# Performance work log

Hardware: AMD Instinct MI355X
Metric: run time of the kernel (lower is better)

Reference implementation:

```python
import jax, jax.numpy as jnp
import numpy as np

S, B, T = 512, 256, 128


def setup_inputs() -> dict:
    key = jax.random.key(0)
    k1, k2, k3, k4, k5, k6 = jax.random.split(key, 6)
    emissions = jax.random.normal(k1, (S, B, T), dtype=jnp.float32)
    # realistic monotone mask: each sequence has a random length in [1, S]
    lengths = jax.random.randint(k2, (B,), 1, S + 1)
    mask = (jnp.arange(S)[:, None] < lengths[None, :]).astype(jnp.float32)  # [S,B]
    tags = jax.random.randint(k3, (S, B), 0, T)
    transitions = jax.random.normal(k4, (T, T), dtype=jnp.float32)
    start_transitions = jax.random.normal(k5, (T,), dtype=jnp.float32)
    stop_transitions = jax.random.normal(k6, (T,), dtype=jnp.float32)
    return {
        "emissions": emissions,
        "mask": mask,
        "tags": tags,
        "transitions": transitions,
        "start_transitions": start_transitions,
        "stop_transitions": stop_transitions,
    }


def reference(emissions, mask, tags, transitions, start_transitions, stop_transitions):
    seq_len, batch, num_tags = emissions.shape

    # ---- log-partition (forward algorithm) + viterbi score, fused scan ----
    init = start_transitions + emissions[0]  # [B,T]

    def part_step(carry, xs):
        fv, vv = carry  # forward var, viterbi var: [B,T]
        em, m = xs      # em: [B,T], m: [B]
        # scores[b, j, k] = em[b, j] + transitions[j, k]  (j=next tag, k=prev tag)
        scores = em[:, :, None] + transitions[None, :, :]          # [B,T,T]
        lse = jax.nn.logsumexp(fv[:, None, :] + scores, axis=2)     # [B,T]
        vmax = jnp.max(vv[:, None, :] + scores, axis=2)             # [B,T]
        fv = m[:, None] * lse + (1.0 - m)[:, None] * fv
        vv = m[:, None] * vmax + (1.0 - m)[:, None] * vv
        return (fv, vv), None

    (fv, vv), _ = jax.lax.scan(part_step, (init, init), (emissions[1:], mask[1:]))
    total_score = jax.nn.logsumexp(fv + stop_transitions, axis=1)   # [B]
    best_path_score = jnp.max(vv + stop_transitions, axis=1)        # [B]

    # ---- gold path score ----
    barange = jnp.arange(batch)
    tag0 = tags[0]
    rps0 = start_transitions[tag0] + emissions[0, barange, tag0] * mask[0]

    def rp_step(carry, xs):
        rps, prev = carry
        cur, em, m = xs  # cur:[B] int, em:[B,T], m:[B]
        rps = rps + transitions[prev, cur] * m
        rps = rps + jnp.take_along_axis(em, cur[:, None], axis=1)[:, 0] * m
        prev = jnp.where(m == 1.0, cur, prev)
        return (rps, prev), None

    (rps, prev), _ = jax.lax.scan(rp_step, (rps0, tag0), (tags[1:], emissions[1:], mask[1:]))
    real_path_score = rps + stop_transitions[prev]

    loss = jnp.mean(total_score - real_path_score)
    return loss, real_path_score, total_score, best_path_score
```

## Files before the change

### kernel.cpp

```cpp
#include <hip/hip_runtime.h>
#include <math.h>

#define S_LEN 512
#define BATCH 256
#define NTAG  128
#define EMSTRIDE (BATCH * NTAG)

typedef float f32x4 __attribute__((ext_vector_type(4)));
typedef float f32x2 __attribute__((ext_vector_type(2)));

__device__ __forceinline__ int lidx(int k) { return k + ((k >> 6) << 2); }
__device__ __forceinline__ f32x2 lo2(f32x4 v){ f32x2 r; r[0]=v[0]; r[1]=v[1]; return r; }
__device__ __forceinline__ f32x2 hi2(f32x4 v){ f32x2 r; r[0]=v[2]; r[1]=v[3]; return r; }
__device__ __forceinline__ f32x2 pmax2(f32x2 a, f32x2 b){
  f32x2 r; r[0]=fmaxf(a[0],b[0]); r[1]=fmaxf(a[1],b[1]); return r;
}

#define DPP_XOR1(x) __int_as_float(__builtin_amdgcn_mov_dpp(__float_as_int(x), 0xB1, 0xF, 0xF, false))

#define BAR() do {                                       \
    asm volatile("s_waitcnt lgkmcnt(0)" ::: "memory");   \
    __builtin_amdgcn_s_barrier();                        \
    __builtin_amdgcn_sched_barrier(0);                   \
  } while (0)

__global__ __launch_bounds__(256, 1)
void crf_fat_kernel(const float* __restrict__ emis,
                    const float* __restrict__ mask,
                    const int* __restrict__ tags,
                    const float* __restrict__ trans,
                    const float* __restrict__ startt,
                    const float* __restrict__ stopt,
                    float* __restrict__ ws,
                    int* __restrict__ ewbuf,
                    float* __restrict__ out)
{
  const int blk  = blockIdx.x;
  const int tid  = threadIdx.x;
  const int role = blk >> 8;
  const int b    = blk & 255;
  const int lane = tid & 63;
  const int wid  = tid >> 6;

  __shared__ __align__(16) float sbuf[2][144];
  __shared__ float red[8];

  if (role == 4) {
    float part = 0.f, lenp = 0.f;
#pragma unroll
    for (int rep = 0; rep < 2; ++rep) {
      int s = tid + rep * 256;
      float m  = mask[(size_t)s * BATCH + b];
      int  cur = tags[(size_t)s * BATCH + b];
      if (s == 0) {
        part += startt[cur] + emis[(size_t)b * NTAG + cur] * m;
      } else {
        int prev = tags[(size_t)(s - 1) * BATCH + b];
        part += m * (trans[(size_t)prev * NTAG + cur] +
                     emis[((size_t)s * BATCH + b) * NTAG + cur]);
      }
      lenp += m;
    }
#pragma unroll
    for (int d = 1; d <= 32; d <<= 1) {
      part += __shfl_xor(part, d);
      lenp += __shfl_xor(lenp, d);
    }
    if (lane == 0) { red[wid] = part; red[4 + wid] = lenp; }
    __syncthreads();
    if (tid == 0) {
      float rps = (red[0] + red[1]) + (red[2] + red[3]);
      float lf  = (red[4] + red[5]) + (red[6] + red[7]);
      int len = (int)(lf + 0.5f);
      int pf  = tags[(size_t)(len - 1) * BATCH + b];
      out[1 + b] = rps + stopt[pf];
    }
    return;
  }

  const int p    = tid >> 1;
  const int h    = tid & 1;
  const int widx = lidx(p);

  int len;
  {
    float mv = mask[(size_t)tid * BATCH + b] +
               mask[(size_t)(tid + 256) * BATCH + b];
#pragma unroll
    for (int d = 1; d <= 32; d <<= 1) mv += __shfl_xor(mv, d);
    if (lane == 0) red[wid] = mv;
    __syncthreads();
    float ls = (red[0] + red[1]) + (red[2] + red[3]);
    len = (int)(ls + 0.5f);
    len = __builtin_amdgcn_readfirstlane(len);
  }
  const int sm     = (len - 1) >> 1;
  const int nsteps = len - 1 - sm;
  const float* eb  = emis + (size_t)b * NTAG + p;

  if (role == 0) {
    f32x2 E2[32];
    {
      const float* tr = trans + (size_t)p * NTAG + 64 * h;
#pragma unroll
      for (int c = 0; c < 16; ++c) {
        f32x4 t = *(const f32x4*)(tr + 4 * c);
        f32x2 a, bb;
        a[0] = __expf(t[0]); a[1] = __expf(t[1]);
        bb[0] = __expf(t[2]); bb[1] = __expf(t[3]);
        E2[2*c] = a; E2[2*c+1] = bb;
      }
    }
    if (h == 0) sbuf[0][widx] = __expf(startt[p] + eb[0]);
    float e0 = eb[(size_t)1 * EMSTRIDE];
    float e1 = eb[(size_t)2 * EMSTRIDE];
    float e2 = eb[(size_t)3 * EMSTRIDE];
    float e3 = eb[(size_t)4 * EMSTRIDE];
    int Ew = 0, fin = 0;
    __syncthreads();

#define FSTEP(U, EXV, RENORM)                                                 \
  {                                                                           \
    if (g + (U) > sm) { fin = (U) & 1; goto epi_f; }                          \
    const f32x4* wr = (const f32x4*)(sbuf[(U) & 1] + 68 * h);                 \
    f32x2 a0 = {0.f, 0.f}, a1 = {0.f, 0.f}, r2 = {0.f, 0.f};                  \
    _Pragma("unroll")                                                         \
    for (int c = 0; c < 16; ++c) {                                            \
      f32x4 w = wr[c];                                                        \
      f32x2 wl = lo2(w), wh = hi2(w);                                         \
      a0 = a0 + E2[2*c] * wl;                                                 \
      a1 = a1 + E2[2*c+1] * wh;                                               \
      if (RENORM) r2 = pmax2(r2, pmax2(wl, wh));                              \
    }                                                                         \
    f32x2 as = a0 + a1;                                                       \
    float sum = as[0] + as[1];                                                \
    sum += DPP_XOR1(sum);                                                     \
    float uf;                                                                 \
    if (RENORM) {                                                             \
      float rw = fmaxf(r2[0], r2[1]);                                         \
      rw = fmaxf(rw, DPP_XOR1(rw));                                           \
      int ew = (int)((__float_as_uint(rw) >> 23) & 0xFF) - 126;               \
      Ew += ew;                                                               \
      float swc = __uint_as_float((unsigned)(127 - ew) << 23);                \
      uf = (EXV) * sum * swc;                                                 \
    } else {                                                                  \
      uf = (EXV) * sum;                                                       \
    }                                                                         \
    if (h == 0) sbuf[((U) + 1) & 1][widx] = uf;                               \
    BAR();                                                                    \
  }

    for (int g = 1; g < S_LEN; g += 4) {
      int c0 = g + 4 < S_LEN ? g + 4 : S_LEN - 1;
      int c1 = g + 5 < S_LEN ? g + 5 : S_LEN - 1;
      int c2 = g + 6 < S_LEN ? g + 6 : S_LEN - 1;
      int c3 = g + 7 < S_LEN ? g + 7 : S_LEN - 1;
      float n0 = eb[(size_t)c0 * EMSTRIDE];
      float n1 = eb[(size_t)c1 * EMSTRIDE];
      float n2 = eb[(size_t)c2 * EMSTRIDE];
      float n3 = eb[(size_t)c3 * EMSTRIDE];
      float x0 = __expf(e0), x1 = __expf(e1);
      float x2 = __expf(e2), x3 = __expf(e3);
      FSTEP(0, x0, 0)
      FSTEP(1, x1, 0)
      FSTEP(2, x2, 0)
      FSTEP(3, x3, 1)
      e0 = n0; e1 = n1; e2 = n2; e3 = n3;
    }
    fin = 0;
epi_f:
    {
      if (tid < 128) ws[(size_t)b * 512 + tid] = sbuf[fin][lidx(tid)];
      if (tid == 0) ewbuf[b] = Ew;
    }
  } else if (role == 1) {
    f32x2 E2[32];
    {
      const float* tc = trans + p + (size_t)(64 * h) * NTAG;
#pragma unroll
      for (int e = 0; e < 32; ++e) {
        f32x2 a;
        a[0] = __expf(tc[(size_t)(2*e)     * NTAG]);
        a[1] = __expf(tc[(size_t)(2*e + 1) * NTAG]);
        E2[e] = a;
      }
    }
    if (h == 0) {
      float st = stopt[p];
      float y = (nsteps > 0) ? __expf(st + eb[(size_t)(len - 1) * EMSTRIDE])
                             : __expf(st);
      sbuf[0][widx] = y;
    }
    int s0i = len - 2;     s0i = s0i < 0 ? 0 : s0i;
    int s1i = len - 3;     s1i = s1i < 0 ? 0 : s1i;
    int s2i = len - 4;     s2i = s2i < 0 ? 0 : s2i;
    int s3i = len - 5;     s3i = s3i < 0 ? 0 : s3i;
    float e0 = eb[(size_t)s0i * EMSTRIDE];
    float e1 = eb[(size_t)s1i * EMSTRIDE];
    float e2 = eb[(size_t)s2i * EMSTRIDE];
    float e3 = eb[(size_t)s3i * EMSTRIDE];
    int Ew = 0, fin = 0;
    __syncthreads();

#define BSTEP(U, EXV, RENORM)                                                 \
  {                                                                           \
    if (gi + (U) >= nsteps) { fin = (U) & 1; goto epi_b; }                    \
    const f32x4* wr = (const f32x4*)(sbuf[(U) & 1] + 68 * h);                 \
    f32x2 a0 = {0.f, 0.f}, a1 = {0.f, 0.f}, r2 = {0.f, 0.f};                  \
    _Pragma("unroll")                                                         \
    for (int c = 0; c < 16; ++c) {                                            \
      f32x4 w = wr[c];                                                        \
      f32x2 wl = lo2(w), wh = hi2(w);                                         \
      a0 = a0 + E2[2*c] * wl;                                                 \
      a1 = a1 + E2[2*c+1] * wh;                                               \
      if (RENORM) r2 = pmax2(r2, pmax2(wl, wh));                              \
    }                                                                         \
    f32x2 as = a0 + a1;                                                       \
    float sum = as[0] + as[1];                                                \
    sum += DPP_XOR1(sum);                                                     \
    float exm = (gi + (U) == nsteps - 1) ? 1.0f : (EXV);                      \
    float uf;                                                                 \
    if (RENORM) {                                                             \
      float rw = fmaxf(r2[0], r2[1]);                                         \
      rw = fmaxf(rw, DPP_XOR1(rw));                                           \
      int ew = (int)((__float_as_uint(rw) >> 23) & 0xFF) - 126;               \
      Ew += ew;                                                               \
      float swc = __uint_as_float((unsigned)(127 - ew) << 23);                \
      uf = exm * sum * swc;                                                   \
    } else {                                                                  \
      uf = exm * sum;                                                         \
    }                                                                         \
    if (h == 0) sbuf[((U) + 1) & 1][widx] = uf;                               \
    BAR();                                                                    \
  }

    for (int gi = 0; gi < S_LEN; gi += 4) {
      int c0 = len - 2 - (gi + 4); c0 = c0 < 0 ? 0 : c0;
      int c1 = len - 2 - (gi + 5); c1 = c1 < 0 ? 0 : c1;
      int c2 = len - 2 - (gi + 6); c2 = c2 < 0 ? 0 : c2;
      int c3 = len - 2 - (gi + 7); c3 = c3 < 0 ? 0 : c3;
      float n0 = eb[(size_t)c0 * EMSTRIDE];
      float n1 = eb[(size_t)c1 * EMSTRIDE];
      float n2 = eb[(size_t)c2 * EMSTRIDE];
      float n3 = eb[(size_t)c3 * EMSTRIDE];
      float x0 = __expf(e0), x1 = __expf(e1);
      float x2 = __expf(e2), x3 = __expf(e3);
      BSTEP(0, x0, 0)
      BSTEP(1, x1, 0)
      BSTEP(2, x2, 0)
      BSTEP(3, x3, 1)
      e0 = n0; e1 = n1; e2 = n2; e3 = n3;
    }
    fin = 0;
epi_b:
    {
      if (tid < 128) ws[(size_t)b * 512 + 128 + tid] = sbuf[fin][lidx(tid)];
      if (tid == 0) ewbuf[BATCH + b] = Ew;
    }
  } else if (role == 2) {
    f32x2 T2[32];
    {
      const float* tr = trans + (size_t)p * NTAG + 64 * h;
#pragma unroll
      for (int c = 0; c < 16; ++c) {
        f32x4 t = *(const f32x4*)(tr + 4 * c);
        T2[2*c]   = lo2(t);
        T2[2*c+1] = hi2(t);
      }
    }
    if (h == 0) sbuf[0][widx] = startt[p] + eb[0];
    float e0 = eb[(size_t)1 * EMSTRIDE];
    float e1 = eb[(size_t)2 * EMSTRIDE];
    float e2 = eb[(size_t)3 * EMSTRIDE];
    float e3 = eb[(size_t)4 * EMSTRIDE];
    int fin = 0;
    __syncthreads();

#define VSTEP(U, EMV)                                                         \
  {                                                                           \
    if (g + (U) > sm) { fin = (U) & 1; goto epi_v; }                          \
    const f32x4* vr = (const f32x4*)(sbuf[(U) & 1] + 68 * h);                 \
    f32x2 m2 = {-3.0e38f, -3.0e38f};                                          \
    _Pragma("unroll")                                                         \
    for (int c = 0; c < 16; ++c) {                                            \
      f32x4 v = vr[c];                                                        \
      m2 = pmax2(m2, pmax2(lo2(v) + T2[2*c], hi2(v) + T2[2*c+1]));            \
    }                                                                         \
    float vm = fmaxf(m2[0], m2[1]);                                           \
    vm = fmaxf(vm, DPP_XOR1(vm));                                             \
    float uv = (EMV) + vm;                                                    \
    if (h == 0) sbuf[((U) + 1) & 1][widx] = uv;                               \
    BAR();                                                                    \
  }

    for (int g = 1; g < S_LEN; g += 4) {
      int c0 = g + 4 < S_LEN ? g + 4 : S_LEN - 1;
      int c1 = g + 5 < S_LEN ? g + 5 : S_LEN - 1;
      int c2 = g + 6 < S_LEN ? g + 6 : S_LEN - 1;
      int c3 = g + 7 < S_LEN ? g + 7 : S_LEN - 1;
      float n0 = eb[(size_t)c0 * EMSTRIDE];
      float n1 = eb[(size_t)c1 * EMSTRIDE];
      float n2 = eb[(size_t)c2 * EMSTRIDE];
      float n3 = eb[(size_t)c3 * EMSTRIDE];
      VSTEP(0, e0)
      VSTEP(1, e1)
      VSTEP(2, e2)
      VSTEP(3, e3)
      e0 = n0; e1 = n1; e2 = n2; e3 = n3;
    }
    fin = 0;
epi_v:
    {
      if (tid < 128) ws[(size_t)b * 512 + 256 + tid] = sbuf[fin][lidx(tid)];
    }
  } else {
    f32x2 T2[32];
    {
      const float* tc = trans + p + (size_t)(64 * h) * NTAG;
#pragma unroll
      for (int e = 0; e < 32; ++e) {
        f32x2 a;
        a[0] = tc[(size_t)(2*e)     * NTAG];
        a[1] = tc[(size_t)(2*e + 1) * NTAG];
        T2[e] = a;
      }
    }
    if (h == 0) {
      float st = stopt[p];
      float y = (nsteps > 0) ? st + eb[(size_t)(len - 1) * EMSTRIDE] : st;
      sbuf[0][widx] = y;
    }
    int s0i = len - 2;     s0i = s0i < 0 ? 0 : s0i;
    int s1i = len - 3;     s1i = s1i < 0 ? 0 : s1i;
    int s2i = len - 4;     s2i = s2i < 0 ? 0 : s2i;
    int s3i = len - 5;     s3i = s3i < 0 ? 0 : s3i;
    float e0 = eb[(size_t)s0i * EMSTRIDE];
    float e1 = eb[(size_t)s1i * EMSTRIDE];
    float e2 = eb[(size_t)s2i * EMSTRIDE];
    float e3 = eb[(size_t)s3i * EMSTRIDE];
    int fin = 0;
    __syncthreads();

#define WSTEP(U, EMV)                                                         \
  {                                                                           \
    if (gi + (U) >= nsteps) { fin = (U) & 1; goto epi_w; }                    \
    const f32x4* vr = (const f32x4*)(sbuf[(U) & 1] + 68 * h);                 \
    f32x2 m2 = {-3.0e38f, -3.0e38f};                                          \
    _Pragma("unroll")                                                         \
    for (int c = 0; c < 16; ++c) {                                            \
      f32x4 v = vr[c];                                                        \
      m2 = pmax2(m2, pmax2(lo2(v) + T2[2*c], hi2(v) + T2[2*c+1]));            \
    }                                                                         \
    float vm = fmaxf(m2[0], m2[1]);                                           \
    vm = fmaxf(vm, DPP_XOR1(vm));                                             \
    float uv = (gi + (U) == nsteps - 1) ? vm : vm + (EMV);                    \
    if (h == 0) sbuf[((U) + 1) & 1][widx] = uv;                               \
    BAR();                                                                    \
  }

    for (int gi = 0; gi < S_LEN; gi += 4) {
      int c0 = len - 2 - (gi + 4); c0 = c0 < 0 ? 0 : c0;
      int c1 = len - 2 - (gi + 5); c1 = c1 < 0 ? 0 : c1;
      int c2 = len - 2 - (gi + 6); c2 = c2 < 0 ? 0 : c2;
      int c3 = len - 2 - (gi + 7); c3 = c3 < 0 ? 0 : c3;
      float n0 = eb[(size_t)c0 * EMSTRIDE];
      float n1 = eb[(size_t)c1 * EMSTRIDE];
      float n2 = eb[(size_t)c2 * EMSTRIDE];
      float n3 = eb[(size_t)c3 * EMSTRIDE];
      WSTEP(0, e0)
      WSTEP(1, e1)
      WSTEP(2, e2)
      WSTEP(3, e3)
      e0 = n0; e1 = n1; e2 = n2; e3 = n3;
    }
    fin = 0;
epi_w:
    {
      if (tid < 128) ws[(size_t)b * 512 + 384 + tid] = sbuf[fin][lidx(tid)];
    }
  }
}

__global__ __launch_bounds__(128, 1)
void crf_combine_kernel(const float* __restrict__ ws,
                        const int* __restrict__ ewbuf,
                        float* __restrict__ out)
{
  const int b = blockIdx.x, k = threadIdx.x;
  const float* base = ws + (size_t)b * 512;
  float t1 = base[k] * base[128 + k];
  float m1 = base[256 + k] + base[384 + k];
#pragma unroll
  for (int d = 1; d <= 32; d <<= 1) {
    t1 += __shfl_xor(t1, d);
    m1 = fmaxf(m1, __shfl_xor(m1, d));
  }
  __shared__ float rs[2], rm[2];
  const int lane = k & 63, wid = k >> 6;
  if (lane == 0) { rs[wid] = t1; rm[wid] = m1; }
  __syncthreads();
  if (k == 0) {
    const double LN2 = 0.6931471805599453;
    int Et = ewbuf[b] + ewbuf[BATCH + b];
    out[1 + BATCH + b]     = (float)((double)Et * LN2 + (double)__logf(rs[0] + rs[1]));
    out[1 + 2 * BATCH + b] = fmaxf(rm[0], rm[1]);
  }
}

__global__ __launch_bounds__(256, 1)
void crf_loss_kernel(float* __restrict__ out)
{
  const int tid = threadIdx.x;
  float dft = out[1 + BATCH + tid] - out[1 + tid];
#pragma unroll
  for (int d = 1; d <= 32; d <<= 1) dft += __shfl_xor(dft, d);
  __shared__ float rs[4];
  const int lane = tid & 63, wid = tid >> 6;
  if (lane == 0) rs[wid] = dft;
  __syncthreads();
  if (tid == 0)
    out[0] = ((rs[0] + rs[1]) + (rs[2] + rs[3])) * (1.0f / BATCH);
}

extern "C" void kernel_launch(void* const* d_in, const int* in_sizes, int n_in,
                              void* d_out, int out_size, void* d_ws, size_t ws_size,
                              hipStream_t stream)
{
  const float* emis   = (const float*)d_in[0];
  const float* mask   = (const float*)d_in[1];
  const int*   tags   = (const int*)d_in[2];
  const float* trans  = (const float*)d_in[3];
  const float* startt = (const float*)d_in[4];
  const float* stopt  = (const float*)d_in[5];
  float* out = (float*)d_out;

  float* wsf   = (float*)d_ws;
  int*   ewbuf = (int*)(wsf + 512 * BATCH);

  crf_fat_kernel<<<5 * BATCH, 256, 0, stream>>>(emis, mask, tags, trans,
                                                startt, stopt, wsf, ewbuf, out);
  crf_combine_kernel<<<BATCH, 128, 0, stream>>>(wsf, ewbuf, out);
  crf_loss_kernel<<<1, 256, 0, stream>>>(out);
}
```

Measured before the change: 210.0 us.

## Shrink recurrence blocks to 128 threads, each lane computing four output tags

Each recurrence block now runs two wavefronts instead of four. Every thread computes partial sums for four output tags over a 32-wide slice of the previous tags, reduces across four lanes with two DPP steps, and selects its own result, so every thread writes one tag per step instead of half the threads idling on the write. The shared-memory padding layout is changed to fit 32-element chunks, and the inner products use explicit FMAs. The intent is to make the per-step barrier cheaper with fewer waves and to reuse each LDS read across four outputs. The cost is more registers per thread (four transition rows held at once) and extra DPP reduction and select work on every step.

New measurement: 213.0 us. No clear change (+1.4%).

```diff
diff --git a/kernel.cpp b/kernel.cpp
--- a/kernel.cpp
+++ b/kernel.cpp
@@ -9,14 +9,19 @@
 typedef float f32x4 __attribute__((ext_vector_type(4)));
 typedef float f32x2 __attribute__((ext_vector_type(2)));
 
-__device__ __forceinline__ int lidx(int k) { return k + ((k >> 6) << 2); }
+__device__ __forceinline__ int lidx(int k) { return (k & 31) + 36 * (k >> 5); }
+
 __device__ __forceinline__ f32x2 lo2(f32x4 v){ f32x2 r; r[0]=v[0]; r[1]=v[1]; return r; }
 __device__ __forceinline__ f32x2 hi2(f32x4 v){ f32x2 r; r[0]=v[2]; r[1]=v[3]; return r; }
 __device__ __forceinline__ f32x2 pmax2(f32x2 a, f32x2 b){
   f32x2 r; r[0]=fmaxf(a[0],b[0]); r[1]=fmaxf(a[1],b[1]); return r;
 }
+__device__ __forceinline__ f32x2 fma2(f32x2 a, f32x2 b, f32x2 c){
+  f32x2 r; r[0]=__builtin_fmaf(a[0],b[0],c[0]); r[1]=__builtin_fmaf(a[1],b[1],c[1]); return r;
+}
 
 #define DPP_XOR1(x) __int_as_float(__builtin_amdgcn_mov_dpp(__float_as_int(x), 0xB1, 0xF, 0xF, false))
+#define DPP_XOR2(x) __int_as_float(__builtin_amdgcn_mov_dpp(__float_as_int(x), 0x4E, 0xF, 0xF, false))
 
 #define BAR() do {                                       \
     asm volatile("s_waitcnt lgkmcnt(0)" ::: "memory");   \
@@ -24,7 +29,7 @@
     __builtin_amdgcn_sched_barrier(0);                   \
   } while (0)
 
-__global__ __launch_bounds__(256, 1)
+__global__ __launch_bounds__(128, 1)
 void crf_fat_kernel(const float* __restrict__ emis,
                     const float* __restrict__ mask,
                     const int* __restrict__ tags,
@@ -48,8 +53,8 @@
   if (role == 4) {
     float part = 0.f, lenp = 0.f;
 #pragma unroll
-    for (int rep = 0; rep < 2; ++rep) {
-      int s = tid + rep * 256;
+    for (int rep = 0; rep < 4; ++rep) {
+      int s = tid + rep * 128;
       float m  = mask[(size_t)s * BATCH + b];
       int  cur = tags[(size_t)s * BATCH + b];
       if (s == 0) {
@@ -66,52 +71,54 @@
       part += __shfl_xor(part, d);
       lenp += __shfl_xor(lenp, d);
     }
-    if (lane == 0) { red[wid] = part; red[4 + wid] = lenp; }
+    if (lane == 0) { red[wid] = part; red[2 + wid] = lenp; }
     __syncthreads();
     if (tid == 0) {
-      float rps = (red[0] + red[1]) + (red[2] + red[3]);
-      float lf  = (red[4] + red[5]) + (red[6] + red[7]);
-      int len = (int)(lf + 0.5f);
+      float rps = red[0] + red[1];
+      int len = (int)(red[2] + red[3] + 0.5f);
       int pf  = tags[(size_t)(len - 1) * BATCH + b];
       out[1 + b] = rps + stopt[pf];
     }
     return;
   }
 
-  const int p    = tid >> 1;
-  const int h    = tid & 1;
-  const int widx = lidx(p);
+  const int h    = tid & 3;
+  const int g    = tid >> 2;
+  const int bch  = 9 * h;
+  const int wloc = lidx(tid);
 
   int len;
   {
     float mv = mask[(size_t)tid * BATCH + b] +
-               mask[(size_t)(tid + 256) * BATCH + b];
+               mask[(size_t)(tid + 128) * BATCH + b] +
+               mask[(size_t)(tid + 256) * BATCH + b] +
+               mask[(size_t)(tid + 384) * BATCH + b];
 #pragma unroll
     for (int d = 1; d <= 32; d <<= 1) mv += __shfl_xor(mv, d);
     if (lane == 0) red[wid] = mv;
     __syncthreads();
-    float ls = (red[0] + red[1]) + (red[2] + red[3]);
-    len = (int)(ls + 0.5f);
+    len = (int)(red[0] + red[1] + 0.5f);
     len = __builtin_amdgcn_readfirstlane(len);
   }
   const int sm     = (len - 1) >> 1;
   const int nsteps = len - 1 - sm;
-  const float* eb  = emis + (size_t)b * NTAG + p;
+  const float* eb  = emis + (size_t)b * NTAG + tid;
 
   if (role == 0) {
-    f32x2 E2[32];
-    {
-      const float* tr = trans + (size_t)p * NTAG + 64 * h;
-#pragma unroll
-      for (int c = 0; c < 16; ++c) {
+    f32x2 E2[4][16];
+#pragma unroll
+    for (int rr = 0; rr < 4; ++rr) {
+      const float* tr = trans + (size_t)(4 * g + rr) * NTAG + 32 * h;
+#pragma unroll
+      for (int c = 0; c < 8; ++c) {
         f32x4 t = *(const f32x4*)(tr + 4 * c);
         f32x2 a, bb;
-        a[0] = __expf(t[0]); a[1] = __expf(t[1]);
+        a[0] = __expf(t[0]);  a[1] = __expf(t[1]);
         bb[0] = __expf(t[2]); bb[1] = __expf(t[3]);
-        E2[2*c] = a; E2[2*c+1] = bb;
+        E2[rr][2*c] = a; E2[rr][2*c+1] = bb;
       }
     }
-    if (h == 0) sbuf[0][widx] = __expf(startt[p] + eb[0]);
+    sbuf[0][wloc] = __expf(startt[tid] + eb[0]);
     float e0 = eb[(size_t)1 * EMSTRIDE];
     float e1 = eb[(size_t)2 * EMSTRIDE];
     float e2 = eb[(size_t)3 * EMSTRIDE];
@@ -119,82 +126,88 @@
     int Ew = 0, fin = 0;
     __syncthreads();
 
-#define FSTEP(U, EXV, RENORM)                                                 \
+#define FSTEP(U, EMV, RENORM)                                                 \
   {                                                                           \
-    if (g + (U) > sm) { fin = (U) & 1; goto epi_f; }                          \
-    const f32x4* wr = (const f32x4*)(sbuf[(U) & 1] + 68 * h);                 \
-    f32x2 a0 = {0.f, 0.f}, a1 = {0.f, 0.f}, r2 = {0.f, 0.f};                  \
+    if (g4 + (U) > sm) { fin = (U) & 1; goto epi_f; }                         \
+    const f32x4* wr = (const f32x4*)sbuf[(U) & 1];                            \
+    f32x2 a0={0.f,0.f}, a1={0.f,0.f}, a2={0.f,0.f}, a3={0.f,0.f};             \
+    f32x2 r2={0.f,0.f};                                                       \
     _Pragma("unroll")                                                         \
-    for (int c = 0; c < 16; ++c) {                                            \
-      f32x4 w = wr[c];                                                        \
+    for (int c = 0; c < 8; ++c) {                                             \
+      f32x4 w = wr[bch + c];                                                  \
       f32x2 wl = lo2(w), wh = hi2(w);                                         \
-      a0 = a0 + E2[2*c] * wl;                                                 \
-      a1 = a1 + E2[2*c+1] * wh;                                               \
+      a0 = fma2(E2[0][2*c], wl, a0); a0 = fma2(E2[0][2*c+1], wh, a0);         \
+      a1 = fma2(E2[1][2*c], wl, a1); a1 = fma2(E2[1][2*c+1], wh, a1);         \
+      a2 = fma2(E2[2][2*c], wl, a2); a2 = fma2(E2[2][2*c+1], wh, a2);         \
+      a3 = fma2(E2[3][2*c], wl, a3); a3 = fma2(E2[3][2*c+1], wh, a3);         \
       if (RENORM) r2 = pmax2(r2, pmax2(wl, wh));                              \
     }                                                                         \
-    f32x2 as = a0 + a1;                                                       \
-    float sum = as[0] + as[1];                                                \
-    sum += DPP_XOR1(sum);                                                     \
+    float s0 = a0[0]+a0[1], s1 = a1[0]+a1[1];                                 \
+    float s2 = a2[0]+a2[1], s3 = a3[0]+a3[1];                                 \
+    s0 += DPP_XOR1(s0); s0 += DPP_XOR2(s0);                                   \
+    s1 += DPP_XOR1(s1); s1 += DPP_XOR2(s1);                                   \
+    s2 += DPP_XOR1(s2); s2 += DPP_XOR2(s2);                                   \
+    s3 += DPP_XOR1(s3); s3 += DPP_XOR2(s3);                                   \
+    float v01 = (h & 1) ? s1 : s0;                                            \
+    float v23 = (h & 1) ? s3 : s2;                                            \
+    float vs  = (h & 2) ? v23 : v01;                                          \
+    float ex  = __expf(EMV);                                                  \
     float uf;                                                                 \
     if (RENORM) {                                                             \
       float rw = fmaxf(r2[0], r2[1]);                                         \
-      rw = fmaxf(rw, DPP_XOR1(rw));                                           \
+      rw = fmaxf(rw, DPP_XOR1(rw)); rw = fmaxf(rw, DPP_XOR2(rw));             \
       int ew = (int)((__float_as_uint(rw) >> 23) & 0xFF) - 126;               \
       Ew += ew;                                                               \
       float swc = __uint_as_float((unsigned)(127 - ew) << 23);                \
-      uf = (EXV) * sum * swc;                                                 \
+      uf = ex * vs * swc;                                                     \
     } else {                                                                  \
-      uf = (EXV) * sum;                                                       \
-    }                                                                         \
-    if (h == 0) sbuf[((U) + 1) & 1][widx] = uf;                               \
+      uf = ex * vs;                                                           \
+    }                                                                         \
+    sbuf[((U) + 1) & 1][wloc] = uf;                                           \
     BAR();                                                                    \
   }
 
-    for (int g = 1; g < S_LEN; g += 4) {
-      int c0 = g + 4 < S_LEN ? g + 4 : S_LEN - 1;
-      int c1 = g + 5 < S_LEN ? g + 5 : S_LEN - 1;
-      int c2 = g + 6 < S_LEN ? g + 6 : S_LEN - 1;
-      int c3 = g + 7 < S_LEN ? g + 7 : S_LEN - 1;
+    for (int g4 = 1; g4 < S_LEN; g4 += 4) {
+      int c0 = g4 + 4 < S_LEN ? g4 + 4 : S_LEN - 1;
+      int c1 = g4 + 5 < S_LEN ? g4 + 5 : S_LEN - 1;
+      int c2 = g4 + 6 < S_LEN ? g4 + 6 : S_LEN - 1;
+      int c3 = g4 + 7 < S_LEN ? g4 + 7 : S_LEN - 1;
       float n0 = eb[(size_t)c0 * EMSTRIDE];
       float n1 = eb[(size_t)c1 * EMSTRIDE];
       float n2 = eb[(size_t)c2 * EMSTRIDE];
       float n3 = eb[(size_t)c3 * EMSTRIDE];
-      float x0 = __expf(e0), x1 = __expf(e1);
-      float x2 = __expf(e2), x3 = __expf(e3);
-      FSTEP(0, x0, 0)
-      FSTEP(1, x1, 0)
-      FSTEP(2, x2, 0)
-      FSTEP(3, x3, 1)
+      FSTEP(0, e0, 0)
+      FSTEP(1, e1, 0)
+      FSTEP(2, e2, 0)
+      FSTEP(3, e3, 1)
       e0 = n0; e1 = n1; e2 = n2; e3 = n3;
     }
     fin = 0;
 epi_f:
+    ws[(size_t)b * 512 + tid] = sbuf[fin][wloc];
+    if (tid == 0) ewbuf[b] = Ew;
+  } else if (role == 1) {
+    f32x2 E2[4][16];
+#pragma unroll
+    for (int rr = 0; rr < 4; ++rr) {
+      const float* tc = trans + (4 * g + rr) + (size_t)(32 * h) * NTAG;
+#pragma unroll
+      for (int q = 0; q < 16; ++q) {
+        f32x2 a;
+        a[0] = __expf(tc[(size_t)(2*q)     * NTAG]);
+        a[1] = __expf(tc[(size_t)(2*q + 1) * NTAG]);
+        E2[rr][q] = a;
+      }
+    }
     {
-      if (tid < 128) ws[(size_t)b * 512 + tid] = sbuf[fin][lidx(tid)];
-      if (tid == 0) ewbuf[b] = Ew;
-    }
-  } else if (role == 1) {
-    f32x2 E2[32];
-    {
-      const float* tc = trans + p + (size_t)(64 * h) * NTAG;
-#pragma unroll
-      for (int e = 0; e < 32; ++e) {
-        f32x2 a;
-        a[0] = __expf(tc[(size_t)(2*e)     * NTAG]);
-        a[1] = __expf(tc[(size_t)(2*e + 1) * NTAG]);
-        E2[e] = a;
-      }
-    }
-    if (h == 0) {
-      float st = stopt[p];
-      float y = (nsteps > 0) ? __expf(st + eb[(size_t)(len - 1) * EMSTRIDE])
-                             : __expf(st);
-      sbuf[0][widx] = y;
-    }
-    int s0i = len - 2;     s0i = s0i < 0 ? 0 : s0i;
-    int s1i = len - 3;     s1i = s1i < 0 ? 0 : s1i;
-    int s2i = len - 4;     s2i = s2i < 0 ? 0 : s2i;
-    int s3i = len - 5;     s3i = s3i < 0 ? 0 : s3i;
+      float st = stopt[tid];
+      sbuf[0][wloc] = (nsteps > 0) ? __expf(st + eb[(size_t)(len - 1) * EMSTRIDE])
+                                   : __expf(st);
+    }
+    int s0i = len - 2; s0i = s0i < 0 ? 0 : s0i;
+    int s1i = len - 3; s1i = s1i < 0 ? 0 : s1i;
+    int s2i = len - 4; s2i = s2i < 0 ? 0 : s2i;
+    int s3i = len - 5; s3i = s3i < 0 ? 0 : s3i;
     float e0 = eb[(size_t)s0i * EMSTRIDE];
     float e1 = eb[(size_t)s1i * EMSTRIDE];
     float e2 = eb[(size_t)s2i * EMSTRIDE];
@@ -202,35 +215,45 @@
     int Ew = 0, fin = 0;
     __syncthreads();
 
-#define BSTEP(U, EXV, RENORM)                                                 \
+#define BSTEP(U, EMV, RENORM)                                                 \
   {                                                                           \
     if (gi + (U) >= nsteps) { fin = (U) & 1; goto epi_b; }                    \
-    const f32x4* wr = (const f32x4*)(sbuf[(U) & 1] + 68 * h);                 \
-    f32x2 a0 = {0.f, 0.f}, a1 = {0.f, 0.f}, r2 = {0.f, 0.f};                  \
+    const f32x4* wr = (const f32x4*)sbuf[(U) & 1];                            \
+    f32x2 a0={0.f,0.f}, a1={0.f,0.f}, a2={0.f,0.f}, a3={0.f,0.f};             \
+    f32x2 r2={0.f,0.f};                                                       \
     _Pragma("unroll")                                                         \
-    for (int c = 0; c < 16; ++c) {                                            \
-      f32x4 w = wr[c];                                                        \
+    for (int c = 0; c < 8; ++c) {                                             \
+      f32x4 w = wr[bch + c];                                                  \
       f32x2 wl = lo2(w), wh = hi2(w);                                         \
-      a0 = a0 + E2[2*c] * wl;                                                 \
-      a1 = a1 + E2[2*c+1] * wh;                                               \
+      a0 = fma2(E2[0][2*c], wl, a0); a0 = fma2(E2[0][2*c+1], wh, a0);         \
+      a1 = fma2(E2[1][2*c], wl, a1); a1 = fma2(E2[1][2*c+1], wh, a1);         \
+      a2 = fma2(E2[2][2*c], wl, a2); a2 = fma2(E2[2][2*c+1], wh, a2);         \
+      a3 = fma2(E2[3][2*c], wl, a3); a3 = fma2(E2[3][2*c+1], wh, a3);         \
       if (RENORM) r2 = pmax2(r2, pmax2(wl, wh));                              \
     }                                                                         \
-    f32x2 as = a0 + a1;                                                       \
-    float sum = as[0] + as[1];                                                \
-    sum += DPP_XOR1(sum);                                                     \
-    float exm = (gi + (U) == nsteps - 1) ? 1.0f : (EXV);                      \
+    float s0 = a0[0]+a0[1], s1 = a1[0]+a1[1];                                 \
+    float s2 = a2[0]+a2[1], s3 = a3[0]+a3[1];                                 \
+    s0 += DPP_XOR1(s0); s0 += DPP_XOR2(s0);                                   \
+    s1 += DPP_XOR1(s1); s1 += DPP_XOR2(s1);                                   \
+    s2 += DPP_XOR1(s2); s2 += DPP_XOR2(s2);                                   \
+    s3 += DPP_XOR1(s3); s3 += DPP_XOR2(s3);                                   \
+    float v01 = (h & 1) ? s1 : s0;                                            \
+    float v23 = (h & 1) ? s3 : s2;                                            \
+    float vs  = (h & 2) ? v23 : v01;                                          \
+    float ex  = __expf(EMV);                                                  \
+    float exm = (gi + (U) == nsteps - 1) ? 1.0f : ex;                         \
     float uf;                                                                 \
     if (RENORM) {                                                             \
       float rw = fmaxf(r2[0], r2[1]);                                         \
-      rw = fmaxf(rw, DPP_XOR1(rw));                                           \
+      rw = fmaxf(rw, DPP_XOR1(rw)); rw = fmaxf(rw, DPP_XOR2(rw));             \
       int ew = (int)((__float_as_uint(rw) >> 23) & 0xFF) - 126;               \
       Ew += ew;                                                               \
       float swc = __uint_as_float((unsigned)(127 - ew) << 23);                \
-      uf = exm * sum * swc;                                                   \
+      uf = exm * vs * swc;                                                    \
     } else {                                                                  \
-      uf = exm * sum;                                                         \
-    }                                                                         \
-    if (h == 0) sbuf[((U) + 1) & 1][widx] = uf;                               \
+      uf = exm * vs;                                                          \
+    }                                                                         \
+    sbuf[((U) + 1) & 1][wloc] = uf;                                           \
     BAR();                                                                    \
   }
 
@@ -243,32 +266,29 @@
       float n1 = eb[(size_t)c1 * EMSTRIDE];
       float n2 = eb[(size_t)c2 * EMSTRIDE];
       float n3 = eb[(size_t)c3 * EMSTRIDE];
-      float x0 = __expf(e0), x1 = __expf(e1);
-      float x2 = __expf(e2), x3 = __expf(e3);
-      BSTEP(0, x0, 0)
-      BSTEP(1, x1, 0)
-      BSTEP(2, x2, 0)
-      BSTEP(3, x3, 1)
+      BSTEP(0, e0, 0)
+      BSTEP(1, e1, 0)
+      BSTEP(2, e2, 0)
+      BSTEP(3, e3, 1)
       e0 = n0; e1 = n1; e2 = n2; e3 = n3;
     }
     fin = 0;
 epi_b:
-    {
-      if (tid < 128) ws[(size_t)b * 512 + 128 + tid] = sbuf[fin][lidx(tid)];
-      if (tid == 0) ewbuf[BATCH + b] = Ew;
-    }
+    ws[(size_t)b * 512 + 128 + tid] = sbuf[fin][wloc];
+    if (tid == 0) ewbuf[BATCH + b] = Ew;
   } else if (role == 2) {
-    f32x2 T2[32];
-    {
-      const float* tr = trans + (size_t)p * NTAG + 64 * h;
-#pragma unroll
-      for (int c = 0; c < 16; ++c) {
+    f32x2 T2[4][16];
+#pragma unroll
+    for (int rr = 0; rr < 4; ++rr) {
+      const float* tr = trans + (size_t)(4 * g + rr) * NTAG + 32 * h;
+#pragma unroll
+      for (int c = 0; c < 8; ++c) {
         f32x4 t = *(const f32x4*)(tr + 4 * c);
-        T2[2*c]   = lo2(t);
-        T2[2*c+1] = hi2(t);
+        T2[rr][2*c]   = lo2(t);
+        T2[rr][2*c+1] = hi2(t);
       }
     }
-    if (h == 0) sbuf[0][widx] = startt[p] + eb[0];
+    sbuf[0][wloc] = startt[tid] + eb[0];
     float e0 = eb[(size_t)1 * EMSTRIDE];
     float e1 = eb[(size_t)2 * EMSTRIDE];
     float e2 = eb[(size_t)3 * EMSTRIDE];
@@ -278,26 +298,37 @@
 
 #define VSTEP(U, EMV)                                                         \
   {                                                                           \
-    if (g + (U) > sm) { fin = (U) & 1; goto epi_v; }                          \
-    const f32x4* vr = (const f32x4*)(sbuf[(U) & 1] + 68 * h);                 \
-    f32x2 m2 = {-3.0e38f, -3.0e38f};                                          \
+    if (g4 + (U) > sm) { fin = (U) & 1; goto epi_v; }                         \
+    const f32x4* vr = (const f32x4*)sbuf[(U) & 1];                            \
+    f32x2 m0={-3.0e38f,-3.0e38f}, m1={-3.0e38f,-3.0e38f};                     \
+    f32x2 m2={-3.0e38f,-3.0e38f}, m3={-3.0e38f,-3.0e38f};                     \
     _Pragma("unroll")                                                         \
-    for (int c = 0; c < 16; ++c) {                                            \
-      f32x4 v = vr[c];                                                        \
-      m2 = pmax2(m2, pmax2(lo2(v) + T2[2*c], hi2(v) + T2[2*c+1]));            \
-    }                                                                         \
-    float vm = fmaxf(m2[0], m2[1]);                                           \
-    vm = fmaxf(vm, DPP_XOR1(vm));                                             \
-    float uv = (EMV) + vm;                                                    \
-    if (h == 0) sbuf[((U) + 1) & 1][widx] = uv;                               \
+    for (int c = 0; c < 8; ++c) {                                             \
+      f32x4 v = vr[bch + c];                                                  \
+      f32x2 vl = lo2(v), vh = hi2(v);                                         \
+      m0 = pmax2(m0, vl + T2[0][2*c]); m0 = pmax2(m0, vh + T2[0][2*c+1]);     \
+      m1 = pmax2(m1, vl + T2[1][2*c]); m1 = pmax2(m1, vh + T2[1][2*c+1]);     \
+      m2 = pmax2(m2, vl + T2[2][2*c]); m2 = pmax2(m2, vh + T2[2][2*c+1]);     \
+      m3 = pmax2(m3, vl + T2[3][2*c]); m3 = pmax2(m3, vh + T2[3][2*c+1]);     \
+    }                                                                         \
+    float s0 = fmaxf(m0[0], m0[1]), s1 = fmaxf(m1[0], m1[1]);                 \
+    float s2 = fmaxf(m2[0], m2[1]), s3 = fmaxf(m3[0], m3[1]);                 \
+    s0 = fmaxf(s0, DPP_XOR1(s0)); s0 = fmaxf(s0, DPP_XOR2(s0));               \
+    s1 = fmaxf(s1, DPP_XOR1(s1)); s1 = fmaxf(s1, DPP_XOR2(s1));               \
+    s2 = fmaxf(s2, DPP_XOR1(s2)); s2 = fmaxf(s2, DPP_XOR2(s2));               \
+    s3 = fmaxf(s3, DPP_XOR1(s3)); s3 = fmaxf(s3, DPP_XOR2(s3));               \
+    float v01 = (h & 1) ? s1 : s0;                                            \
+    float v23 = (h & 1) ? s3 : s2;                                            \
+    float vs  = (h & 2) ? v23 : v01;                                          \
+    sbuf[((U) + 1) & 1][wloc] = (EMV) + vs;                                   \
     BAR();                                                                    \
   }
 
-    for (int g = 1; g < S_LEN; g += 4) {
-      int c0 = g + 4 < S_LEN ? g + 4 : S_LEN - 1;
-      int c1 = g + 5 < S_LEN ? g + 5 : S_LEN - 1;
-      int c2 = g + 6 < S_LEN ? g + 6 : S_LEN - 1;
-      int c3 = g + 7 < S_LEN ? g + 7 : S_LEN - 1;
+    for (int g4 = 1; g4 < S_LEN; g4 += 4) {
+      int c0 = g4 + 4 < S_LEN ? g4 + 4 : S_LEN - 1;
+      int c1 = g4 + 5 < S_LEN ? g4 + 5 : S_LEN - 1;
+      int c2 = g4 + 6 < S_LEN ? g4 + 6 : S_LEN - 1;
+      int c3 = g4 + 7 < S_LEN ? g4 + 7 : S_LEN - 1;
       float n0 = eb[(size_t)c0 * EMSTRIDE];
       float n1 = eb[(size_t)c1 * EMSTRIDE];
       float n2 = eb[(size_t)c2 * EMSTRIDE];
@@ -310,30 +341,28 @@
     }
     fin = 0;
 epi_v:
+    ws[(size_t)b * 512 + 256 + tid] = sbuf[fin][wloc];
+  } else {
+    f32x2 T2[4][16];
+#pragma unroll
+    for (int rr = 0; rr < 4; ++rr) {
+      const float* tc = trans + (4 * g + rr) + (size_t)(32 * h) * NTAG;
+#pragma unroll
+      for (int q = 0; q < 16; ++q) {
+        f32x2 a;
+        a[0] = tc[(size_t)(2*q)     * NTAG];
+        a[1] = tc[(size_t)(2*q + 1) * NTAG];
+        T2[rr][q] = a;
+      }
+    }
     {
-      if (tid < 128) ws[(size_t)b * 512 + 256 + tid] = sbuf[fin][lidx(tid)];
-    }
-  } else {
-    f32x2 T2[32];
-    {
-      const float* tc = trans + p + (size_t)(64 * h) * NTAG;
-#pragma unroll
-      for (int e = 0; e < 32; ++e) {
-        f32x2 a;
-        a[0] = tc[(size_t)(2*e)     * NTAG];
-        a[1] = tc[(size_t)(2*e + 1) * NTAG];
-        T2[e] = a;
-      }
-    }
-    if (h == 0) {
-      float st = stopt[p];
-      float y = (nsteps > 0) ? st + eb[(size_t)(len - 1) * EMSTRIDE] : st;
-      sbuf[0][widx] = y;
-    }
-    int s0i = len - 2;     s0i = s0i < 0 ? 0 : s0i;
-    int s1i = len - 3;     s1i = s1i < 0 ? 0 : s1i;
-    int s2i = len - 4;     s2i = s2i < 0 ? 0 : s2i;
-    int s3i = len - 5;     s3i = s3i < 0 ? 0 : s3i;
+      float st = stopt[tid];
+      sbuf[0][wloc] = (nsteps > 0) ? st + eb[(size_t)(len - 1) * EMSTRIDE] : st;
+    }
+    int s0i = len - 2; s0i = s0i < 0 ? 0 : s0i;
+    int s1i = len - 3; s1i = s1i < 0 ? 0 : s1i;
+    int s2i = len - 4; s2i = s2i < 0 ? 0 : s2i;
+    int s3i = len - 5; s3i = s3i < 0 ? 0 : s3i;
     float e0 = eb[(size_t)s0i * EMSTRIDE];
     float e1 = eb[(size_t)s1i * EMSTRIDE];
     float e2 = eb[(size_t)s2i * EMSTRIDE];
@@ -344,17 +373,29 @@
 #define WSTEP(U, EMV)                                                         \
   {                                                                           \
     if (gi + (U) >= nsteps) { fin = (U) & 1; goto epi_w; }                    \
-    const f32x4* vr = (const f32x4*)(sbuf[(U) & 1] + 68 * h);                 \
-    f32x2 m2 = {-3.0e38f, -3.0e38f};                                          \
+    const f32x4* vr = (const f32x4*)sbuf[(U) & 1];                            \
+    f32x2 m0={-3.0e38f,-3.0e38f}, m1={-3.0e38f,-3.0e38f};                     \
+    f32x2 m2={-3.0e38f,-3.0e38f}, m3={-3.0e38f,-3.0e38f};                     \
     _Pragma("unroll")                                                         \
-    for (int c = 0; c < 16; ++c) {                                            \
-      f32x4 v = vr[c];                                                        \
-      m2 = pmax2(m2, pmax2(lo2(v) + T2[2*c], hi2(v) + T2[2*c+1]));            \
-    }                                                                         \
-    float vm = fmaxf(m2[0], m2[1]);                                           \
-    vm = fmaxf(vm, DPP_XOR1(vm));                                             \
-    float uv = (gi + (U) == nsteps - 1) ? vm : vm + (EMV);                    \
-    if (h == 0) sbuf[((U) + 1) & 1][widx] = uv;                               \
+    for (int c = 0; c < 8; ++c) {                                             \
+      f32x4 v = vr[bch + c];                                                  \
+      f32x2 vl = lo2(v), vh = hi2(v);                                         \
+      m0 = pmax2(m0, vl + T2[0][2*c]); m0 = pmax2(m0, vh + T2[0][2*c+1]);     \
+      m1 = pmax2(m1, vl + T2[1][2*c]); m1 = pmax2(m1, vh + T2[1][2*c+1]);     \
+      m2 = pmax2(m2, vl + T2[2][2*c]); m2 = pmax2(m2, vh + T2[2][2*c+1]);     \
+      m3 = pmax2(m3, vl + T2[3][2*c]); m3 = pmax2(m3, vh + T2[3][2*c+1]);     \
+    }                                                                         \
+    float s0 = fmaxf(m0[0], m0[1]), s1 = fmaxf(m1[0], m1[1]);                 \
+    float s2 = fmaxf(m2[0], m2[1]), s3 = fmaxf(m3[0], m3[1]);                 \
+    s0 = fmaxf(s0, DPP_XOR1(s0)); s0 = fmaxf(s0, DPP_XOR2(s0));               \
+    s1 = fmaxf(s1, DPP_XOR1(s1)); s1 = fmaxf(s1, DPP_XOR2(s1));               \
+    s2 = fmaxf(s2, DPP_XOR1(s2)); s2 = fmaxf(s2, DPP_XOR2(s2));               \
+    s3 = fmaxf(s3, DPP_XOR1(s3)); s3 = fmaxf(s3, DPP_XOR2(s3));               \
+    float v01 = (h & 1) ? s1 : s0;                                            \
+    float v23 = (h & 1) ? s3 : s2;                                            \
+    float vs  = (h & 2) ? v23 : v01;                                          \
+    float uv  = (gi + (U) == nsteps - 1) ? vs : vs + (EMV);                   \
+    sbuf[((U) + 1) & 1][wloc] = uv;                                           \
     BAR();                                                                    \
   }
 
@@ -375,9 +416,7 @@
     }
     fin = 0;
 epi_w:
-    {
-      if (tid < 128) ws[(size_t)b * 512 + 384 + tid] = sbuf[fin][lidx(tid)];
-    }
+    ws[(size_t)b * 512 + 384 + tid] = sbuf[fin][wloc];
   }
 }
 
@@ -437,7 +476,7 @@
   float* wsf   = (float*)d_ws;
   int*   ewbuf = (int*)(wsf + 512 * BATCH);
 
-  crf_fat_kernel<<<5 * BATCH, 256, 0, stream>>>(emis, mask, tags, trans,
+  crf_fat_kernel<<<5 * BATCH, 128, 0, stream>>>(emis, mask, tags, trans,
                                                 startt, stopt, wsf, ewbuf, out);
   crf_combine_kernel<<<BATCH, 128, 0, stream>>>(wsf, ewbuf, out);
   crf_loss_kernel<<<1, 256, 0, stream>>>(out);
```
